# Kernel tuning notes

Measured on AMD Instinct MI355X. Metric: run time of the kernel, lower is better.

Reference implementation:

```python
import jax, jax.numpy as jnp
import numpy as np

DIM, NHEADS, HEAD_DIM = 1536, 12, 128
EPS = 1e-6
ROPE_SPLIT = (22, 21, 21)  # head_dim//2 = 64 -> (c-2*(c//3), c//3, c//3)


def setup_inputs() -> dict:
    key = jax.random.key(0)
    ks = jax.random.split(key, 12)
    B, F, H, W = 1, 8, 16, 28
    L = F * H * W  # 3584
    inp = {
        "x": jax.random.normal(ks[0], (B, L, DIM), jnp.float32),
        "seq_lens": jnp.full((B,), L, dtype=jnp.int64),
        "grid_sizes": jnp.array([[F, H, W]] * B, dtype=jnp.int64),
        "freqs": jax.random.uniform(ks[1], (1024, HEAD_DIM // 2), jnp.float32) * (2 * np.pi),
        "Wq": jax.random.normal(ks[2], (DIM, DIM), jnp.float32) / np.sqrt(DIM),
        "bq": jnp.zeros((DIM,), jnp.float32),
        "Wk": jax.random.normal(ks[3], (DIM, DIM), jnp.float32) / np.sqrt(DIM),
        "bk": jnp.zeros((DIM,), jnp.float32),
        "Wv": jax.random.normal(ks[4], (DIM, DIM), jnp.float32) / np.sqrt(DIM),
        "bv": jnp.zeros((DIM,), jnp.float32),
        "Wo": jax.random.normal(ks[5], (DIM, DIM), jnp.float32) / np.sqrt(DIM),
        "bo": jnp.zeros((DIM,), jnp.float32),
        "gq": jnp.ones((DIM,), jnp.float32),
        "gk": jnp.ones((DIM,), jnp.float32),
    }
    return inp


def _rms_norm(x, g):
    var = jnp.mean(jnp.square(x), axis=-1, keepdims=True)
    return x * jax.lax.rsqrt(var + EPS) * g


def _rope_angles(freqs, F, H, W):
    # freqs: [1024, 64] angles; split per 3D axis and broadcast over the grid
    cf, ch, cw = ROPE_SPLIT
    af = freqs[:F, :cf]
    ah = freqs[:H, cf:cf + ch]
    aw = freqs[:W, cf + ch:]
    ang = jnp.concatenate([
        jnp.broadcast_to(af[:, None, None, :], (F, H, W, cf)),
        jnp.broadcast_to(ah[None, :, None, :], (F, H, W, ch)),
        jnp.broadcast_to(aw[None, None, :, :], (F, H, W, cw)),
    ], axis=-1).reshape(F * H * W, cf + ch + cw)  # [L, 64]
    return jnp.cos(ang), jnp.sin(ang)


def _rope_apply(x, cos, sin):
    # x: [B, L, N, D]; complex multiply by unit-modulus freqs, in real arithmetic
    b, s, n, d = x.shape
    xr = x.reshape(b, s, n, d // 2, 2)
    a, bi = xr[..., 0], xr[..., 1]
    c = cos[None, :, None, :]
    si = sin[None, :, None, :]
    out = jnp.stack([a * c - bi * si, a * si + bi * c], axis=-1)
    return out.reshape(b, s, n, d)


def reference(x, seq_lens, grid_sizes, freqs, Wq, bq, Wk, bk, Wv, bv, Wo, bo, gq, gk):
    b, s, _ = x.shape
    n, d = NHEADS, HEAD_DIM
    gs = np.asarray(grid_sizes)
    F, H, W = int(gs[0, 0]), int(gs[0, 1]), int(gs[0, 2])  # static grid (same per batch)

    q = _rms_norm(x @ Wq + bq, gq).reshape(b, s, n, d)
    k = _rms_norm(x @ Wk + bk, gk).reshape(b, s, n, d)
    v = (x @ Wv + bv).reshape(b, s, n, d)

    cos, sin = _rope_angles(freqs, F, H, W)
    q = _rope_apply(q, cos, sin)
    k = _rope_apply(k, cos, sin)

    # full attention with key-length masking (flash_attention k_lens semantics)
    scale = 1.0 / np.sqrt(d)
    scores = jnp.einsum("bqnd,bknd->bnqk", q, k) * scale
    key_mask = jnp.arange(s)[None, :] < seq_lens[:, None]  # [B, S]
    scores = jnp.where(key_mask[:, None, None, :], scores, -1e9)
    probs = jax.nn.softmax(scores, axis=-1)
    out = jnp.einsum("bnqk,bknd->bqnd", probs, v)

    return out.reshape(b, s, n * d) @ Wo + bo
```

## Files before the change

### kernel.cpp

```cpp
#include <hip/hip_runtime.h>

typedef __bf16 bf16;
typedef __bf16 bf16x8 __attribute__((ext_vector_type(8)));
typedef __bf16 bf16x4 __attribute__((ext_vector_type(4)));
typedef float f32x4 __attribute__((ext_vector_type(4)));

__device__ __forceinline__ void gload_lds16(const void* g, void* l) {
  __builtin_amdgcn_global_load_lds(
      (const __attribute__((address_space(1))) void*)g,
      (__attribute__((address_space(3))) void*)l, 16, 0, 0);
}

__device__ __forceinline__ bf16x8 ld8(const bf16* p) {
  bf16x8 v; __builtin_memcpy(&v, p, 16); return v;
}

__global__ __launch_bounds__(256) void cast_f32_bf16(const float* __restrict__ in,
                                                     bf16* __restrict__ out, int n8) {
  int i = blockIdx.x * 256 + threadIdx.x;
  if (i >= n8) return;
  const float4* p = (const float4*)in + (size_t)i * 2;
  float4 a = p[0], b = p[1];
  bf16x8 o;
  o[0] = (bf16)a.x; o[1] = (bf16)a.y; o[2] = (bf16)a.z; o[3] = (bf16)a.w;
  o[4] = (bf16)b.x; o[5] = (bf16)b.y; o[6] = (bf16)b.z; o[7] = (bf16)b.w;
  *((bf16x8*)out + i) = o;
}

__global__ __launch_bounds__(256) void transpose_w(const float* __restrict__ W,
                                                   bf16* __restrict__ Wt) {
  __shared__ bf16 tile[64][72];
  int t = threadIdx.x;
  int k0 = blockIdx.x * 64, n0 = blockIdx.y * 64;
  int r = t >> 2, c0 = (t & 3) * 16;
  const float* src = W + (size_t)(k0 + r) * 1536 + n0 + c0;
#pragma unroll
  for (int q = 0; q < 4; ++q) {
    float4 v = *(const float4*)(src + q * 4);
    tile[c0 + q * 4 + 0][r] = (bf16)v.x;
    tile[c0 + q * 4 + 1][r] = (bf16)v.y;
    tile[c0 + q * 4 + 2][r] = (bf16)v.z;
    tile[c0 + q * 4 + 3][r] = (bf16)v.w;
  }
  __syncthreads();
  bf16* dst = Wt + (size_t)(n0 + r) * 1536 + k0 + c0;
  bf16x8 o0, o1;
#pragma unroll
  for (int j = 0; j < 8; ++j) { o0[j] = tile[r][c0 + j]; o1[j] = tile[r][c0 + 8 + j]; }
  *(bf16x8*)dst = o0;
  *(bf16x8*)(dst + 8) = o1;
}

__global__ void concat_bias(const float* __restrict__ bq, const float* __restrict__ bk,
                            const float* __restrict__ bv, float* __restrict__ o) {
  int t = blockIdx.x * 256 + threadIdx.x;
  if (t < 1536) o[t] = bq[t];
  else if (t < 3072) o[t] = bk[t - 1536];
  else if (t < 4608) o[t] = bv[t - 3072];
}

template <typename OUT>
__global__ __launch_bounds__(256, 2) void gemm_bt(const bf16* __restrict__ A, const bf16* __restrict__ B,
                                                  const float* __restrict__ bias, OUT* __restrict__ C,
                                                  int M, int N, int K) {
  __shared__ bf16 As[128 * 32], Bs[128 * 32];
  int t = threadIdx.x, l = t & 63, w = t >> 6;
  int lane15 = l & 15, lhi = l >> 4;
  int m0 = blockIdx.x * 128, n0 = blockIdx.y * 128;
  int wm = (w >> 1) * 64, wn = (w & 1) * 64;
  f32x4 zero = {0.f, 0.f, 0.f, 0.f};
  f32x4 acc[4][4];
#pragma unroll
  for (int i = 0; i < 4; ++i)
#pragma unroll
    for (int j = 0; j < 4; ++j) acc[i][j] = zero;

  int srow = t >> 2, scol = (t & 3) * 8;
  const bf16* gA0 = A + (size_t)(m0 + srow) * K + scol;
  const bf16* gA1 = A + (size_t)(m0 + 64 + srow) * K + scol;
  const bf16* gB0 = B + (size_t)(n0 + srow) * K + scol;
  const bf16* gB1 = B + (size_t)(n0 + 64 + srow) * K + scol;
  char* ldsA = (char*)As + (size_t)w * 1024;
  char* ldsB = (char*)Bs + (size_t)w * 1024;

  for (int kt = 0; kt < K; kt += 32) {
    gload_lds16(gA0 + kt, ldsA);
    gload_lds16(gA1 + kt, ldsA + 4096);
    gload_lds16(gB0 + kt, ldsB);
    gload_lds16(gB1 + kt, ldsB + 4096);
    __syncthreads();
    bf16x8 af[4], bfr[4];
#pragma unroll
    for (int i = 0; i < 4; ++i) {
      af[i]  = ld8(&As[(wm + i * 16 + lane15) * 32 + lhi * 8]);
      bfr[i] = ld8(&Bs[(wn + i * 16 + lane15) * 32 + lhi * 8]);
    }
#pragma unroll
    for (int i = 0; i < 4; ++i)
#pragma unroll
      for (int j = 0; j < 4; ++j)
        acc[i][j] = __builtin_amdgcn_mfma_f32_16x16x32_bf16(af[i], bfr[j], acc[i][j], 0, 0, 0);
    __syncthreads();
  }
#pragma unroll
  for (int i = 0; i < 4; ++i)
#pragma unroll
    for (int j = 0; j < 4; ++j) {
      int col = n0 + wn + j * 16 + lane15;
      float bb = bias[col];
#pragma unroll
      for (int r = 0; r < 4; ++r) {
        int row = m0 + wm + i * 16 + lhi * 4 + r;
        C[(size_t)row * N + col] = (OUT)(acc[i][j][r] + bb);
      }
    }
}

__global__ void rope_tab(const float* __restrict__ freqs, const int* __restrict__ gs,
                         float* __restrict__ tabc, float* __restrict__ tabs) {
  int idx = blockIdx.x * 256 + threadIdx.x;
  if (idx >= 3584 * 64) return;
  int s = idx >> 6, i = idx & 63;
  int H = gs[1], W = gs[2];
  int f = s / (H * W);
  int rem = s - f * (H * W);
  int hh = rem / W;
  int ww = rem - hh * W;
  int row = (i < 22) ? f : ((i < 43) ? hh : ww);
  float a = freqs[row * 64 + i];
  tabc[idx] = cosf(a);
  tabs[idx] = sinf(a);
}

__global__ __launch_bounds__(256) void postproc(const bf16* __restrict__ QKV,
    const float* __restrict__ gq, const float* __restrict__ gk,
    const float* __restrict__ tabc, const float* __restrict__ tabs,
    bf16* __restrict__ qb, bf16* __restrict__ kb) {
  int s = blockIdx.x, t = threadIdx.x;
  const bf16* Qr = QKV + (size_t)s * 4608;
  const bf16* Kr = Qr + 1536;
  int j0 = t * 6;
  float qv[6], kv[6];
  float sq = 0.f, sk = 0.f;
#pragma unroll
  for (int j = 0; j < 6; ++j) {
    float a = (float)Qr[j0 + j]; qv[j] = a; sq += a * a;
    float b = (float)Kr[j0 + j]; kv[j] = b; sk += b * b;
  }
#pragma unroll
  for (int off = 32; off > 0; off >>= 1) {
    sq += __shfl_down(sq, off);
    sk += __shfl_down(sk, off);
  }
  __shared__ float red[2][4];
  if ((t & 63) == 0) { red[0][t >> 6] = sq; red[1][t >> 6] = sk; }
  __syncthreads();
  float vq = (red[0][0] + red[0][1]) + (red[0][2] + red[0][3]);
  float vk = (red[1][0] + red[1][1]) + (red[1][2] + red[1][3]);
  float rq = 1.0f / sqrtf(vq * (1.0f / 1536.0f) + 1e-6f);
  float rk = 1.0f / sqrtf(vk * (1.0f / 1536.0f) + 1e-6f);
  rq *= 0.08838834764831845f;
#pragma unroll
  for (int j = 0; j < 6; j += 2) {
    int jj = j0 + j;
    int d = jj & 127, i = d >> 1, h = jj >> 7;
    float c = tabc[s * 64 + i], sn = tabs[s * 64 + i];
    size_t base = (((size_t)h * 3584 + s) << 7) + d;
    float a = qv[j] * rq * gq[jj], b = qv[j + 1] * rq * gq[jj + 1];
    qb[base] = (bf16)(a * c - b * sn);
    qb[base + 1] = (bf16)(a * sn + b * c);
    float ak = kv[j] * rk * gk[jj], bk2 = kv[j + 1] * rk * gk[jj + 1];
    kb[base] = (bf16)(ak * c - bk2 * sn);
    kb[base + 1] = (bf16)(ak * sn + bk2 * c);
  }
}

__global__ __launch_bounds__(256) void transpose_v(const bf16* __restrict__ QKV,
                                                   bf16* __restrict__ vT) {
  __shared__ bf16 tile[128][72];
  int t = threadIdx.x;
  int h = blockIdx.y;
  int s0 = blockIdx.x * 64;
  int r = t >> 2, c0 = (t & 3) * 32;
  const bf16* src = QKV + (size_t)(s0 + r) * 4608 + 3072 + h * 128 + c0;
#pragma unroll
  for (int q = 0; q < 4; ++q) {
    bf16x8 v = ld8(src + q * 8);
#pragma unroll
    for (int j = 0; j < 8; ++j) tile[c0 + q * 8 + j][r] = v[j];
  }
  __syncthreads();
  int d = t >> 1, spHalf = t & 1;
  bf16* dstBase = vT + (size_t)(h * 128 + d) * 3584 + s0;
#pragma unroll
  for (int q = 0; q < 4; ++q) {
    int mm = spHalf * 4 + q;
    int sA = 32 * (mm >> 2) + 16 * (mm & 1) + 4 * ((mm >> 1) & 1);
    bf16x4 lo, hi;
#pragma unroll
    for (int j = 0; j < 4; ++j) {
      lo[j] = tile[d][spHalf * 32 + q * 8 + j];
      hi[j] = tile[d][spHalf * 32 + q * 8 + 4 + j];
    }
    *(bf16x4*)(dstBase + sA) = lo;
    *(bf16x4*)(dstBase + sA + 8) = hi;
  }
}

__global__ __launch_bounds__(256, 2) void flash_attn(
    const bf16* __restrict__ qb, const bf16* __restrict__ kb, const bf16* __restrict__ vT,
    const int* __restrict__ sl, bf16* __restrict__ po0, bf16* __restrict__ po1,
    bf16* __restrict__ po2, bf16* __restrict__ po3, float* __restrict__ ml) {
  const int L = 3584;
  __shared__ bf16 Ks[64 * 128];
  __shared__ bf16 Vs[128 * 64];
  int t = threadIdx.x, l = t & 63, w = t >> 6;
  int lane15 = l & 15, lhi = l >> 4;
  int grp48 = l & 48;
  int b = blockIdx.x;
  int xcd = b & 7, k_ = b >> 3;
  int pg = k_ / 28, x = k_ - pg * 28;
  int p = pg * 8 + xcd;
  int h = p % 12, z = p / 12;
  int qw = x * 128 + w * 32;
  int seqlen = sl[0];
  bf16* po = (z == 0) ? po0 : (z == 1) ? po1 : (z == 2) ? po2 : po3;
  float* mlz = ml + (size_t)z * 12 * L * 2;

  bf16x8 aq[2][4];
#pragma unroll
  for (int qf = 0; qf < 2; ++qf)
#pragma unroll
    for (int kc = 0; kc < 4; ++kc)
      aq[qf][kc] = ld8(qb + (((size_t)h * L + qw + qf * 16 + lane15) << 7) + kc * 32 + lhi * 8);

  f32x4 zero = {0.f, 0.f, 0.f, 0.f};
  f32x4 out[2][8];
  float m2[2] = {-1e30f, -1e30f}, ls2[2] = {0.f, 0.f};
#pragma unroll
  for (int qf = 0; qf < 2; ++qf)
#pragma unroll
    for (int df = 0; df < 8; ++df) out[qf][df] = zero;

  int nt = (seqlen + 63) >> 6;
  if (nt > 56) nt = 56;
  int t0 = z * 14, t1 = t0 + 14;
  if (t0 > nt) t0 = nt;
  if (t1 > nt) t1 = nt;

  int rk_s = t >> 4, ck_s = (t & 15) * 16;
  int rv_s = t >> 3, cv_s = (t & 7) * 16;
  int swzk = (rk_s & 7) << 4;
  int swzv = (rv_s & 7) << 4;

  bf16x8 kreg[4], vreg[4];
  if (t0 < t1) {
    int kv0 = t0 * 64;
#pragma unroll
    for (int pp = 0; pp < 4; ++pp) {
      kreg[pp] = ld8(kb + (((size_t)h * L + kv0 + pp * 16 + rk_s) << 7) + (ck_s >> 1));
      vreg[pp] = ld8(vT + (size_t)(h * 128 + pp * 32 + rv_s) * L + kv0 + (cv_s >> 1));
    }
  }

  for (int ti = t0; ti < t1; ++ti) {
    int kv0 = ti * 64;
#pragma unroll
    for (int pp = 0; pp < 4; ++pp) {
      __builtin_memcpy((char*)Ks + (pp * 16 + rk_s) * 256 + (ck_s ^ swzk), &kreg[pp], 16);
      __builtin_memcpy((char*)Vs + (pp * 32 + rv_s) * 128 + (cv_s ^ swzv), &vreg[pp], 16);
    }
    if (ti + 1 < t1) {
      int kn = (ti + 1) * 64;
#pragma unroll
      for (int pp = 0; pp < 4; ++pp) {
        kreg[pp] = ld8(kb + (((size_t)h * L + kn + pp * 16 + rk_s) << 7) + (ck_s >> 1));
        vreg[pp] = ld8(vT + (size_t)(h * 128 + pp * 32 + rv_s) * L + kn + (cv_s >> 1));
      }
    }
    __syncthreads();

    f32x4 sc[2][4];
#pragma unroll
    for (int qf = 0; qf < 2; ++qf)
#pragma unroll
      for (int a = 0; a < 4; ++a) sc[qf][a] = zero;
#pragma unroll
    for (int a = 0; a < 4; ++a) {
      int rk = a * 16 + lane15;
      const char* krow = (const char*)Ks + rk * 256;
      int swz = (rk & 7) << 4;
#pragma unroll
      for (int kc = 0; kc < 4; ++kc) {
        bf16x8 bk_ = ld8((const bf16*)(krow + ((kc * 64 + lhi * 16) ^ swz)));
        sc[0][a] = __builtin_amdgcn_mfma_f32_16x16x32_bf16(bk_, aq[0][kc], sc[0][a], 0, 0, 0);
        sc[1][a] = __builtin_amdgcn_mfma_f32_16x16x32_bf16(bk_, aq[1][kc], sc[1][a], 0, 0, 0);
      }
    }

    bool full = (kv0 + 64 <= seqlen);
    bf16x8 ap[2][2];
#pragma unroll
    for (int qf = 0; qf < 2; ++qf) {
      float tm = -1e30f;
#pragma unroll
      for (int a = 0; a < 4; ++a)
#pragma unroll
        for (int r = 0; r < 4; ++r) {
          float s = sc[qf][a][r];
          if (!full) {
            int col = kv0 + a * 16 + lhi * 4 + r;
            s = (col < seqlen) ? s : -1e30f;
            sc[qf][a][r] = s;
          }
          tm = fmaxf(tm, s);
        }
      tm = fmaxf(tm, __shfl_xor(tm, 16));
      tm = fmaxf(tm, __shfl_xor(tm, 32));
      if (!__all(tm <= m2[qf] + 8.0f)) {
        float nm = fmaxf(m2[qf], tm);
        float f = __expf(m2[qf] - nm);
        m2[qf] = nm;
        ls2[qf] *= f;
#pragma unroll
        for (int r = 0; r < 4; ++r) {
          float fr = __shfl(f, grp48 | (lhi * 4 + r));
#pragma unroll
          for (int df = 0; df < 8; ++df) out[qf][df][r] *= fr;
        }
      }
      float psum = 0.f;
#pragma unroll
      for (int a = 0; a < 4; ++a)
#pragma unroll
        for (int r = 0; r < 4; ++r) {
          float pv = __expf(sc[qf][a][r] - m2[qf]);
          sc[qf][a][r] = pv;
          psum += pv;
        }
      psum += __shfl_xor(psum, 16);
      psum += __shfl_xor(psum, 32);
      ls2[qf] += psum;
#pragma unroll
      for (int c = 0; c < 2; ++c) {
        bf16x8 f8;
#pragma unroll
        for (int r = 0; r < 4; ++r) {
          f8[r] = (bf16)sc[qf][2 * c][r];
          f8[r + 4] = (bf16)sc[qf][2 * c + 1][r];
        }
        ap[qf][c] = f8;
      }
    }

#pragma unroll
    for (int df = 0; df < 8; ++df) {
      int rd = df * 16 + lane15;
      const char* vrow2 = (const char*)Vs + rd * 128;
      int swz = (rd & 7) << 4;
#pragma unroll
      for (int c = 0; c < 2; ++c) {
        bf16x8 bv_ = ld8((const bf16*)(vrow2 + ((c * 64 + lhi * 16) ^ swz)));
        out[0][df] = __builtin_amdgcn_mfma_f32_16x16x32_bf16(ap[0][c], bv_, out[0][df], 0, 0, 0);
        out[1][df] = __builtin_amdgcn_mfma_f32_16x16x32_bf16(ap[1][c], bv_, out[1][df], 0, 0, 0);
      }
    }
    __syncthreads();
  }

#pragma unroll
  for (int qf = 0; qf < 2; ++qf) {
#pragma unroll
    for (int r = 0; r < 4; ++r) {
      int row = qw + qf * 16 + lhi * 4 + r;
      size_t rbase = ((size_t)h * L + row) << 7;
#pragma unroll
      for (int df = 0; df < 8; ++df)
        po[rbase + df * 16 + lane15] = (bf16)out[qf][df][r];
    }
    if (lhi == 0) {
      int row = qw + qf * 16 + lane15;
      mlz[(((size_t)h * L + row) << 1)] = m2[qf];
      mlz[(((size_t)h * L + row) << 1) + 1] = ls2[qf];
    }
  }
}

__global__ __launch_bounds__(256) void combine4(
    const bf16* __restrict__ po0, const bf16* __restrict__ po1,
    const bf16* __restrict__ po2, const bf16* __restrict__ po3,
    const float* __restrict__ ml, bf16* __restrict__ attn) {
  const int L = 3584;
  int row = blockIdx.x * 8 + (threadIdx.x >> 5);
  int c0 = (threadIdx.x & 31) * 4;
  const size_t mls = (size_t)12 * L * 2;
  float m0 = ml[row * 2],           l0 = ml[row * 2 + 1];
  float m1 = ml[mls + row * 2],     l1 = ml[mls + row * 2 + 1];
  float m2 = ml[2 * mls + row * 2], l2 = ml[2 * mls + row * 2 + 1];
  float m3 = ml[3 * mls + row * 2], l3 = ml[3 * mls + row * 2 + 1];
  float M = fmaxf(fmaxf(m0, m1), fmaxf(m2, m3));
  float w0 = __expf(m0 - M), w1 = __expf(m1 - M);
  float w2 = __expf(m2 - M), w3 = __expf(m3 - M);
  float inv = 1.0f / fmaxf(w0 * l0 + w1 * l1 + w2 * l2 + w3 * l3, 1e-30f);
  bf16x4 a, b, c, d;
  __builtin_memcpy(&a, po0 + (size_t)row * 128 + c0, 8);
  __builtin_memcpy(&b, po1 + (size_t)row * 128 + c0, 8);
  __builtin_memcpy(&c, po2 + (size_t)row * 128 + c0, 8);
  __builtin_memcpy(&d, po3 + (size_t)row * 128 + c0, 8);
  int h = row / L, s = row % L;
  bf16x4 o;
#pragma unroll
  for (int j = 0; j < 4; ++j)
    o[j] = (bf16)((w0 * (float)a[j] + w1 * (float)b[j] + w2 * (float)c[j] + w3 * (float)d[j]) * inv);
  *(bf16x4*)(attn + (size_t)s * 1536 + h * 128 + c0) = o;
}

extern "C" void kernel_launch(void* const* d_in, const int* in_sizes, int n_in,
                              void* d_out, int out_size, void* d_ws, size_t ws_size,
                              hipStream_t stream) {
  const float* x = (const float*)d_in[0];
  const int* seq_lens = (const int*)d_in[1];
  const int* grid_sizes = (const int*)d_in[2];
  const float* freqs = (const float*)d_in[3];
  const float* Wq = (const float*)d_in[4];
  const float* bq = (const float*)d_in[5];
  const float* Wk = (const float*)d_in[6];
  const float* bk = (const float*)d_in[7];
  const float* Wv = (const float*)d_in[8];
  const float* bv = (const float*)d_in[9];
  const float* Wo = (const float*)d_in[10];
  const float* bo = (const float*)d_in[11];
  const float* gq = (const float*)d_in[12];
  const float* gk = (const float*)d_in[13];

  char* ws = (char*)d_ws;
  bf16* x_bf = (bf16*)(ws + 0);
  bf16* wqkvt = (bf16*)(ws + 11010048);
  bf16* wot = (bf16*)(ws + 25165824);
  float* bqkv = (float*)(ws + 29884416);
  bf16* QKV = (bf16*)(ws + 29902848);
  bf16* qb = (bf16*)(ws + 62932992);
  bf16* kb = (bf16*)(ws + 73943040);
  bf16* vT = (bf16*)(ws + 84953088);
  float* tabc = (float*)(ws + 95963136);
  float* tabs = (float*)(ws + 96880640);
  bf16* po0 = (bf16*)(ws + 29902848);
  bf16* attn = (bf16*)(ws + 51922944);
  bf16* po1 = (bf16*)(ws + 0);
  bf16* po2 = (bf16*)(ws + 11010048);
  float* ml  = (float*)(ws + 95963136);
  bf16* po3 = (bf16*)(ws + 97798144);

  cast_f32_bf16<<<2688, 256, 0, stream>>>(x, x_bf, 688128);
  transpose_w<<<dim3(24, 24), 256, 0, stream>>>(Wq, wqkvt);
  transpose_w<<<dim3(24, 24), 256, 0, stream>>>(Wk, wqkvt + 1536 * 1536);
  transpose_w<<<dim3(24, 24), 256, 0, stream>>>(Wv, wqkvt + 2 * 1536 * 1536);
  transpose_w<<<dim3(24, 24), 256, 0, stream>>>(Wo, wot);
  concat_bias<<<18, 256, 0, stream>>>(bq, bk, bv, bqkv);
  rope_tab<<<896, 256, 0, stream>>>(freqs, grid_sizes, tabc, tabs);
  gemm_bt<bf16><<<dim3(28, 36), 256, 0, stream>>>(x_bf, wqkvt, bqkv, QKV, 3584, 4608, 1536);
  postproc<<<3584, 256, 0, stream>>>(QKV, gq, gk, tabc, tabs, qb, kb);
  transpose_v<<<dim3(56, 12), 256, 0, stream>>>(QKV, vT);
  flash_attn<<<1344, 256, 0, stream>>>(qb, kb, vT, seq_lens, po0, po1, po2, po3, ml);
  combine4<<<5376, 256, 0, stream>>>(po0, po1, po2, po3, ml, attn);
  gemm_bt<float><<<dim3(28, 12), 256, 0, stream>>>(attn, wot, bo, (float*)d_out, 3584, 1536, 1536);
}
```

Baseline: 274.4 us.

## Pre-swizzle K/V tiles in global memory and load via direct global-to-LDS

The producer kernels now write K and V^T as contiguous 64-token tile images, with the LDS swizzle already applied. The attention kernel then copies each 16KB tile straight into shared memory with global_load_lds, replacing the register-staged prefetch and separate LDS stores. This removes VGPR pressure and LDS write instructions. The cost is that the next tile's load is no longer overlapped with compute, since the prefetch into registers is dropped and each load is bracketed by barriers.

```diff
diff --git a/kernel.cpp b/kernel.cpp
--- a/kernel.cpp
+++ b/kernel.cpp
@@ -165,13 +165,14 @@
     int jj = j0 + j;
     int d = jj & 127, i = d >> 1, h = jj >> 7;
     float c = tabc[s * 64 + i], sn = tabs[s * 64 + i];
-    size_t base = (((size_t)h * 3584 + s) << 7) + d;
+    size_t qbase = (((size_t)h * 3584 + s) << 7) + d;
     float a = qv[j] * rq * gq[jj], b = qv[j + 1] * rq * gq[jj + 1];
-    qb[base] = (bf16)(a * c - b * sn);
-    qb[base + 1] = (bf16)(a * sn + b * c);
+    qb[qbase] = (bf16)(a * c - b * sn);
+    qb[qbase + 1] = (bf16)(a * sn + b * c);
+    size_t kbase = (((size_t)(h * 56 + (s >> 6)) * 64 + (s & 63)) << 7) + (d ^ ((s & 7) << 3));
     float ak = kv[j] * rk * gk[jj], bk2 = kv[j + 1] * rk * gk[jj + 1];
-    kb[base] = (bf16)(ak * c - bk2 * sn);
-    kb[base + 1] = (bf16)(ak * sn + bk2 * c);
+    kb[kbase] = (bf16)(ak * c - bk2 * sn);
+    kb[kbase + 1] = (bf16)(ak * sn + bk2 * c);
   }
 }
 
@@ -191,7 +192,8 @@
   }
   __syncthreads();
   int d = t >> 1, spHalf = t & 1;
-  bf16* dstBase = vT + (size_t)(h * 128 + d) * 3584 + s0;
+  int sw = (d & 7) << 3;
+  bf16* dstBase = vT + ((size_t)(h * 56 + blockIdx.x) * 128 + d) * 64;
 #pragma unroll
   for (int q = 0; q < 4; ++q) {
     int mm = spHalf * 4 + q;
@@ -202,8 +204,9 @@
       lo[j] = tile[d][spHalf * 32 + q * 8 + j];
       hi[j] = tile[d][spHalf * 32 + q * 8 + 4 + j];
     }
-    *(bf16x4*)(dstBase + sA) = lo;
-    *(bf16x4*)(dstBase + sA + 8) = hi;
+    int slo = sA ^ sw;
+    *(bf16x4*)(dstBase + slo) = lo;
+    *(bf16x4*)(dstBase + (slo ^ 8)) = hi;
   }
 }
 
@@ -248,34 +251,20 @@
   if (t0 > nt) t0 = nt;
   if (t1 > nt) t1 = nt;
 
-  int rk_s = t >> 4, ck_s = (t & 15) * 16;
-  int rv_s = t >> 3, cv_s = (t & 7) * 16;
-  int swzk = (rk_s & 7) << 4;
-  int swzv = (rv_s & 7) << 4;
-
-  bf16x8 kreg[4], vreg[4];
-  if (t0 < t1) {
-    int kv0 = t0 * 64;
-#pragma unroll
-    for (int pp = 0; pp < 4; ++pp) {
-      kreg[pp] = ld8(kb + (((size_t)h * L + kv0 + pp * 16 + rk_s) << 7) + (ck_s >> 1));
-      vreg[pp] = ld8(vT + (size_t)(h * 128 + pp * 32 + rv_s) * L + kv0 + (cv_s >> 1));
-    }
-  }
+  int src_off = w * 1024 + l * 16;
+  char* ksd = (char*)Ks + w * 1024;
+  char* vsd = (char*)Vs + w * 1024;
 
   for (int ti = t0; ti < t1; ++ti) {
     int kv0 = ti * 64;
-#pragma unroll
-    for (int pp = 0; pp < 4; ++pp) {
-      __builtin_memcpy((char*)Ks + (pp * 16 + rk_s) * 256 + (ck_s ^ swzk), &kreg[pp], 16);
-      __builtin_memcpy((char*)Vs + (pp * 32 + rv_s) * 128 + (cv_s ^ swzv), &vreg[pp], 16);
-    }
-    if (ti + 1 < t1) {
-      int kn = (ti + 1) * 64;
+    __syncthreads();
+    {
+      const char* kimg = (const char*)kb + ((size_t)(h * 56) + ti) * 16384;
+      const char* vimg = (const char*)vT + ((size_t)(h * 56) + ti) * 16384;
 #pragma unroll
       for (int pp = 0; pp < 4; ++pp) {
-        kreg[pp] = ld8(kb + (((size_t)h * L + kn + pp * 16 + rk_s) << 7) + (ck_s >> 1));
-        vreg[pp] = ld8(vT + (size_t)(h * 128 + pp * 32 + rv_s) * L + kn + (cv_s >> 1));
+        gload_lds16(kimg + pp * 4096 + src_off, ksd + pp * 4096);
+        gload_lds16(vimg + pp * 4096 + src_off, vsd + pp * 4096);
       }
     }
     __syncthreads();
@@ -365,7 +354,6 @@
         out[1][df] = __builtin_amdgcn_mfma_f32_16x16x32_bf16(ap[1][c], bv_, out[1][df], 0, 0, 0);
       }
     }
-    __syncthreads();
   }
 
 #pragma unroll
```

Result: no change. 274.8 us (+0.2%).
